# Performance work log

Measured on AMD Instinct MI355X. Metric: run time of the kernel, lower is better.

## Reference

```python
import jax, jax.numpy as jnp
import numpy as np

MARGIN = 0.7
SINKHORN_ITERS = 500


def setup_inputs() -> dict:
    key = jax.random.key(0)
    k1, k2, k3, k4, k5 = jax.random.split(key, 5)
    D, m, n = 2048, 2048, 2048
    query_features = jax.random.normal(k1, (D, m), dtype=jnp.float32)
    target_features = jax.random.normal(k2, (D, n), dtype=jnp.float32)
    # positive marginals (mu.log() / nu.log() must be finite), normalized to sum 1
    qa = jax.random.uniform(k3, (m,), dtype=jnp.float32, minval=0.1, maxval=1.0)
    ta = jax.random.uniform(k4, (n,), dtype=jnp.float32, minval=0.1, maxval=1.0)
    query_attention = qa / qa.sum()
    target_attention = ta / ta.sum()
    # contrastive label: 1 = positive pair, 0 = negative
    label = (jax.random.uniform(k5, (m,)) < 0.5).astype(jnp.float32)
    return {
        "query_features": query_features,
        "query_attention": query_attention,
        "target_features": target_features,
        "target_attention": target_attention,
        "label": label,
    }


def _pairwise_sq_dist(x, y):
    # x: [m, D], y: [n, D] -> squared euclidean distances [m, n], clamped at 0
    x2 = jnp.sum(x * x, axis=1)[:, None]
    y2 = jnp.sum(y * y, axis=1)[None, :]
    d = x2 + y2 - 2.0 * (x @ y.T)
    return jnp.maximum(d, 0.0)


def _log_sinkhorn(Z, log_mu, log_nu, iters):
    # Z: [m, n]; log-space Sinkhorn, matching torch version with batch dim squeezed
    u0 = jnp.zeros_like(log_mu)
    v0 = jnp.zeros_like(log_nu)

    def body(_, uv):
        u, v = uv
        u = log_mu - jax.nn.logsumexp(Z + v[None, :], axis=1)
        v = log_nu - jax.nn.logsumexp(Z + u[:, None], axis=0)
        return (u, v)

    u, v = jax.lax.fori_loop(0, iters, body, (u0, v0))
    return Z + u[:, None] + v[None, :]


def reference(query_features, query_attention, target_features, target_attention, label):
    qf = query_features.T  # [m, D]
    tf = target_features.T  # [n, D]
    M = _pairwise_sq_dist(qf, tf)  # [m, n]
    logP = _log_sinkhorn(M, jnp.log(query_attention), jnp.log(target_attention), SINKHORN_ITERS)
    P = jnp.exp(logP)  # [m, n]
    # per-query-descriptor residual between weighted query and OT-transported target
    resid = query_attention[:, None] * qf - P @ tf  # [m, D]
    distance = jnp.linalg.norm(resid, axis=1)  # [m]
    loss = 0.5 * label * distance ** 2 + 0.5 * (1.0 - label) * jnp.maximum(MARGIN - distance, 0.0) ** 2
    return loss.sum()
```

## Files before the change

kernel.cpp:

```cpp
#include <hip/hip_runtime.h>
#include <math.h>

#define S 2048
#define MARGIN 0.7f
#define ITERS 500

__global__ __launch_bounds__(256) void init_marg_k(const float* __restrict__ qa,
                                                   const float* __restrict__ ta,
                                                   float* __restrict__ lmu,
                                                   float* __restrict__ lnu,
                                                   float* __restrict__ vt,
                                                   float* __restrict__ dist2) {
  int i = blockIdx.x * 256 + threadIdx.x;
  lmu[i] = __logf(qa[i]);
  lnu[i] = __logf(ta[i]);
  vt[i] = 0.f;
  dist2[i] = 0.f;
}

__global__ __launch_bounds__(256) void colsumsq_k(const float* __restrict__ TF,
                                                  float* __restrict__ vt) {
  int jb = blockIdx.x & 7, dc = blockIdx.x >> 3;
  int j = jb * 256 + threadIdx.x;
  int d0 = dc * 256;
  float acc = 0.f;
  for (int d = d0; d < d0 + 256; ++d) {
    float v = TF[d * S + j];
    acc = fmaf(v, v, acc);
  }
  atomicAdd(&vt[j], acc);
}

__global__ __launch_bounds__(256) void gemm_tn_k(const float* __restrict__ A,
                                                 const float* __restrict__ B,
                                                 float* __restrict__ C, float alpha) {
  __shared__ float As[16][128];
  __shared__ float Bs[16][128];
  int t = threadIdx.x;
  int i0 = blockIdx.y * 128, j0 = blockIdx.x * 128;
  int tx = t & 15, ty = t >> 4;
  float acc[8][8];
#pragma unroll
  for (int r = 0; r < 8; ++r)
#pragma unroll
    for (int c = 0; c < 8; ++c) acc[r][c] = 0.f;

  int e = t * 4;
  int dd0 = e >> 7, ii = e & 127;
  int dd1 = dd0 + 8;
  for (int k0 = 0; k0 < S; k0 += 16) {
    float4 a0 = *(const float4*)&A[(k0 + dd0) * S + i0 + ii];
    float4 b0 = *(const float4*)&B[(k0 + dd0) * S + j0 + ii];
    float4 a1 = *(const float4*)&A[(k0 + dd1) * S + i0 + ii];
    float4 b1 = *(const float4*)&B[(k0 + dd1) * S + j0 + ii];
    __syncthreads();
    *(float4*)&As[dd0][ii] = a0; *(float4*)&Bs[dd0][ii] = b0;
    *(float4*)&As[dd1][ii] = a1; *(float4*)&Bs[dd1][ii] = b1;
    __syncthreads();
#pragma unroll
    for (int kk = 0; kk < 16; ++kk) {
      float a[8], b[8];
      *(float4*)&a[0] = *(const float4*)&As[kk][ty * 8];
      *(float4*)&a[4] = *(const float4*)&As[kk][ty * 8 + 4];
      *(float4*)&b[0] = *(const float4*)&Bs[kk][tx * 4];
      *(float4*)&b[4] = *(const float4*)&Bs[kk][64 + tx * 4];
#pragma unroll
      for (int r = 0; r < 8; ++r)
#pragma unroll
        for (int c = 0; c < 8; ++c) acc[r][c] = fmaf(a[r], b[c], acc[r][c]);
    }
  }
#pragma unroll
  for (int r = 0; r < 8; ++r) {
    int i = i0 + ty * 8 + r;
    float4 o0 = make_float4(acc[r][0] * alpha, acc[r][1] * alpha, acc[r][2] * alpha, acc[r][3] * alpha);
    float4 o1 = make_float4(acc[r][4] * alpha, acc[r][5] * alpha, acc[r][6] * alpha, acc[r][7] * alpha);
    *(float4*)&C[i * S + j0 + tx * 4] = o0;
    *(float4*)&C[i * S + j0 + 64 + tx * 4] = o1;
  }
}

__global__ __launch_bounds__(256) void transpose_k(const float* __restrict__ in,
                                                   float* __restrict__ out) {
  __shared__ float tile[64][65];
  int i0 = blockIdx.y * 64, j0 = blockIdx.x * 64;
  int tx = threadIdx.x & 63, ty = threadIdx.x >> 6;
#pragma unroll
  for (int r = 0; r < 16; ++r) {
    int row = r * 4 + ty;
    tile[row][tx] = in[(i0 + row) * S + j0 + tx];
  }
  __syncthreads();
#pragma unroll
  for (int r = 0; r < 16; ++r) {
    int row = r * 4 + ty;
    out[(j0 + row) * S + i0 + tx] = tile[tx][row];
  }
}

__global__ __launch_bounds__(256) void lse_update_k(const float* __restrict__ G,
                                                    const float* __restrict__ inPot,
                                                    const float* __restrict__ logMarg,
                                                    float* __restrict__ outPot) {
  __shared__ float red[8];
  int t = threadIdx.x;
  int row = blockIdx.x;
  const float* g = G + (size_t)row * S;
  int idx = t * 8;
  float4 g0 = *(const float4*)&g[idx];
  float4 g1 = *(const float4*)&g[idx + 4];
  float4 p0 = *(const float4*)&inPot[idx];
  float4 p1 = *(const float4*)&inPot[idx + 4];
  float v0 = g0.x + p0.x, v1 = g0.y + p0.y, v2 = g0.z + p0.z, v3 = g0.w + p0.w;
  float v4 = g1.x + p1.x, v5 = g1.y + p1.y, v6 = g1.z + p1.z, v7 = g1.w + p1.w;
  float mx = fmaxf(fmaxf(fmaxf(v0, v1), fmaxf(v2, v3)),
                   fmaxf(fmaxf(v4, v5), fmaxf(v6, v7)));
#pragma unroll
  for (int off = 32; off; off >>= 1) mx = fmaxf(mx, __shfl_xor(mx, off));
  int wave = t >> 6, lane = t & 63;
  if (lane == 0) red[wave] = mx;
  __syncthreads();
  mx = fmaxf(fmaxf(red[0], red[1]), fmaxf(red[2], red[3]));
  float s = __expf(v0 - mx) + __expf(v1 - mx) + __expf(v2 - mx) + __expf(v3 - mx) +
            __expf(v4 - mx) + __expf(v5 - mx) + __expf(v6 - mx) + __expf(v7 - mx);
#pragma unroll
  for (int off = 32; off; off >>= 1) s += __shfl_xor(s, off);
  if (lane == 0) red[4 + wave] = s;
  __syncthreads();
  if (t == 0) {
    s = red[4] + red[5] + red[6] + red[7];
    outPot[row] = logMarg[row] - (mx + __logf(s));
  }
}

__global__ __launch_bounds__(256) void rt_gemm_k(const float* __restrict__ TF,
                                                 const float* __restrict__ GpT,
                                                 const float* __restrict__ ut,
                                                 const float* __restrict__ vt,
                                                 float* __restrict__ RT) {
  __shared__ float As[16][128];
  __shared__ float Bs[16][128];
  int t = threadIdx.x;
  int d0 = blockIdx.y * 128, i0 = blockIdx.x * 128;
  int tx = t & 15, ty = t >> 4;
  float acc[8][8];
#pragma unroll
  for (int r = 0; r < 8; ++r)
#pragma unroll
    for (int c = 0; c < 8; ++c) acc[r][c] = 0.f;

  int akk = (t * 4) & 15, add0 = t >> 2;
  int eb = t * 4;
  int bkk0 = eb >> 7, bii = eb & 127, bkk1 = bkk0 + 8;
  float4 u4 = *(const float4*)&ut[i0 + bii];

  for (int k0 = 0; k0 < S; k0 += 16) {
    float4 av0 = *(const float4*)&TF[(d0 + add0) * S + k0 + akk];
    float4 av1 = *(const float4*)&TF[(d0 + add0 + 64) * S + k0 + akk];
    float4 g0 = *(const float4*)&GpT[(k0 + bkk0) * S + i0 + bii];
    float4 g1 = *(const float4*)&GpT[(k0 + bkk1) * S + i0 + bii];
    float v0 = vt[k0 + bkk0], v1 = vt[k0 + bkk1];
    __syncthreads();
    As[akk + 0][add0] = av0.x; As[akk + 1][add0] = av0.y;
    As[akk + 2][add0] = av0.z; As[akk + 3][add0] = av0.w;
    As[akk + 0][add0 + 64] = av1.x; As[akk + 1][add0 + 64] = av1.y;
    As[akk + 2][add0 + 64] = av1.z; As[akk + 3][add0 + 64] = av1.w;
    float4 p0 = make_float4(__expf(g0.x + u4.x + v0), __expf(g0.y + u4.y + v0),
                            __expf(g0.z + u4.z + v0), __expf(g0.w + u4.w + v0));
    float4 p1 = make_float4(__expf(g1.x + u4.x + v1), __expf(g1.y + u4.y + v1),
                            __expf(g1.z + u4.z + v1), __expf(g1.w + u4.w + v1));
    *(float4*)&Bs[bkk0][bii] = p0;
    *(float4*)&Bs[bkk1][bii] = p1;
    __syncthreads();
#pragma unroll
    for (int kk = 0; kk < 16; ++kk) {
      float a[8], b[8];
      *(float4*)&a[0] = *(const float4*)&As[kk][ty * 8];
      *(float4*)&a[4] = *(const float4*)&As[kk][ty * 8 + 4];
      *(float4*)&b[0] = *(const float4*)&Bs[kk][tx * 4];
      *(float4*)&b[4] = *(const float4*)&Bs[kk][64 + tx * 4];
#pragma unroll
      for (int r = 0; r < 8; ++r)
#pragma unroll
        for (int c = 0; c < 8; ++c) acc[r][c] = fmaf(a[r], b[c], acc[r][c]);
    }
  }
#pragma unroll
  for (int r = 0; r < 8; ++r) {
    int d = d0 + ty * 8 + r;
    *(float4*)&RT[d * S + i0 + tx * 4] = *(float4*)&acc[r][0];
    *(float4*)&RT[d * S + i0 + 64 + tx * 4] = *(float4*)&acc[r][4];
  }
}

__global__ __launch_bounds__(256) void dist2_partial_k(const float* __restrict__ QF,
                                                       const float* __restrict__ RT,
                                                       const float* __restrict__ qa,
                                                       float* __restrict__ dist2) {
  int ib = blockIdx.x & 7, dc = blockIdx.x >> 3;
  int i = ib * 256 + threadIdx.x;
  float qai = qa[i];
  float acc = 0.f;
  int d0 = dc * 256;
  for (int d = d0; d < d0 + 256; ++d) {
    float q = QF[d * S + i];
    float r = RT[d * S + i];
    float x = fmaf(qai, q, -r);
    acc = fmaf(x, x, acc);
  }
  atomicAdd(&dist2[i], acc);
}

__global__ __launch_bounds__(256) void loss_final_k(const float* __restrict__ dist2,
                                                    const float* __restrict__ label,
                                                    float* __restrict__ out) {
  int t = threadIdx.x;
  float acc = 0.f;
#pragma unroll
  for (int k = 0; k < 8; ++k) {
    int i = t + k * 256;
    float d2 = dist2[i];
    float dist = sqrtf(d2);
    float lab = label[i];
    float neg = fmaxf(MARGIN - dist, 0.f);
    acc += 0.5f * lab * d2 + 0.5f * (1.f - lab) * neg * neg;
  }
#pragma unroll
  for (int off = 32; off; off >>= 1) acc += __shfl_xor(acc, off);
  __shared__ float wsum[4];
  int wave = t >> 6, lane = t & 63;
  if (lane == 0) wsum[wave] = acc;
  __syncthreads();
  if (t == 0) out[0] = wsum[0] + wsum[1] + wsum[2] + wsum[3];
}

extern "C" void kernel_launch(void* const* d_in, const int* in_sizes, int n_in,
                              void* d_out, int out_size, void* d_ws, size_t ws_size,
                              hipStream_t stream) {
  const float* QF  = (const float*)d_in[0];
  const float* qa  = (const float*)d_in[1];
  const float* TF  = (const float*)d_in[2];
  const float* ta  = (const float*)d_in[3];
  const float* lab = (const float*)d_in[4];
  float* out = (float*)d_out;

  float* ws = (float*)d_ws;
  float* Gp    = ws;
  float* GpT   = Gp + S * S;
  float* ut    = GpT + S * S;
  float* vt    = ut + S;
  float* lmu   = vt + S;
  float* lnu   = lmu + S;
  float* dist2 = lnu + S;

  init_marg_k<<<8, 256, 0, stream>>>(qa, ta, lmu, lnu, vt, dist2);
  colsumsq_k<<<64, 256, 0, stream>>>(TF, vt);
  gemm_tn_k<<<dim3(16, 16), 256, 0, stream>>>(QF, TF, Gp, -2.0f);
  transpose_k<<<dim3(32, 32), 256, 0, stream>>>(Gp, GpT);

  for (int it = 0; it < ITERS; ++it) {
    lse_update_k<<<2048, 256, 0, stream>>>(Gp, vt, lmu, ut);
    lse_update_k<<<2048, 256, 0, stream>>>(GpT, ut, lnu, vt);
  }

  rt_gemm_k<<<dim3(16, 16), 256, 0, stream>>>(TF, GpT, ut, vt, Gp);
  dist2_partial_k<<<64, 256, 0, stream>>>(QF, Gp, qa, dist2);
  loss_final_k<<<1, 256, 0, stream>>>(dist2, lab, out);
}
```

Baseline: 4.542 ms.

## Replace per-iteration Sinkhorn launches with persistent cooperative kernel and LDS-resident cost rows

```diff
diff --git a/kernel.cpp b/kernel.cpp
--- a/kernel.cpp
+++ b/kernel.cpp
@@ -4,18 +4,25 @@
 #define S 2048
 #define MARGIN 0.7f
 #define ITERS 500
+#define NBLK 256
+#define TPB 512
+#define NGRP 16
 
 __global__ __launch_bounds__(256) void init_marg_k(const float* __restrict__ qa,
                                                    const float* __restrict__ ta,
                                                    float* __restrict__ lmu,
                                                    float* __restrict__ lnu,
                                                    float* __restrict__ vt,
-                                                   float* __restrict__ dist2) {
+                                                   float* __restrict__ dist2,
+                                                   unsigned* __restrict__ grp,
+                                                   unsigned* __restrict__ gbar) {
   int i = blockIdx.x * 256 + threadIdx.x;
   lmu[i] = __logf(qa[i]);
   lnu[i] = __logf(ta[i]);
   vt[i] = 0.f;
   dist2[i] = 0.f;
+  if (i < 512) grp[i] = 0u;
+  if (i == 0) *gbar = 0u;
 }
 
 __global__ __launch_bounds__(256) void colsumsq_k(const float* __restrict__ TF,
@@ -98,38 +105,127 @@
   }
 }
 
-__global__ __launch_bounds__(256) void lse_update_k(const float* __restrict__ G,
-                                                    const float* __restrict__ inPot,
-                                                    const float* __restrict__ logMarg,
-                                                    float* __restrict__ outPot) {
-  __shared__ float red[8];
-  int t = threadIdx.x;
-  int row = blockIdx.x;
-  const float* g = G + (size_t)row * S;
-  int idx = t * 8;
-  float4 g0 = *(const float4*)&g[idx];
-  float4 g1 = *(const float4*)&g[idx + 4];
-  float4 p0 = *(const float4*)&inPot[idx];
-  float4 p1 = *(const float4*)&inPot[idx + 4];
-  float v0 = g0.x + p0.x, v1 = g0.y + p0.y, v2 = g0.z + p0.z, v3 = g0.w + p0.w;
-  float v4 = g1.x + p1.x, v5 = g1.y + p1.y, v6 = g1.z + p1.z, v7 = g1.w + p1.w;
-  float mx = fmaxf(fmaxf(fmaxf(v0, v1), fmaxf(v2, v3)),
-                   fmaxf(fmaxf(v4, v5), fmaxf(v6, v7)));
-#pragma unroll
-  for (int off = 32; off; off >>= 1) mx = fmaxf(mx, __shfl_xor(mx, off));
-  int wave = t >> 6, lane = t & 63;
-  if (lane == 0) red[wave] = mx;
-  __syncthreads();
-  mx = fmaxf(fmaxf(red[0], red[1]), fmaxf(red[2], red[3]));
-  float s = __expf(v0 - mx) + __expf(v1 - mx) + __expf(v2 - mx) + __expf(v3 - mx) +
-            __expf(v4 - mx) + __expf(v5 - mx) + __expf(v6 - mx) + __expf(v7 - mx);
+#define PADD(P, A) P.x += A.x; P.y += A.y; P.z += A.z; P.w += A.w
+#define PMAX(P) fmaxf(fmaxf(P.x, P.y), fmaxf(P.z, P.w))
+#define PEXPS(P) (__expf(P.x - m) + __expf(P.y - m) + __expf(P.z - m) + __expf(P.w - m))
+
+__device__ __forceinline__ void stage_pot(const float* __restrict__ src,
+                                          float* __restrict__ s_pot, int t) {
+  const unsigned long long* s64 = (const unsigned long long*)src;
+  unsigned long long* d64 = (unsigned long long*)s_pot;
+#pragma unroll
+  for (int k = 0; k < 2; ++k) {
+    int idx = t + (k << 9);
+    d64[idx] = __hip_atomic_load(&s64[idx], __ATOMIC_RELAXED,
+                                 __HIP_MEMORY_SCOPE_AGENT);
+  }
+}
+
+__device__ __forceinline__ float lse_row(const float* __restrict__ grow,
+                                         const float* __restrict__ s_pot,
+                                         int lane) {
+  int j0 = lane << 2;
+  float4 p0 = *(const float4*)&s_pot[j0];
+  float4 p1 = *(const float4*)&s_pot[j0 + 256];
+  float4 p2 = *(const float4*)&s_pot[j0 + 512];
+  float4 p3 = *(const float4*)&s_pot[j0 + 768];
+  float4 p4 = *(const float4*)&s_pot[j0 + 1024];
+  float4 p5 = *(const float4*)&s_pot[j0 + 1280];
+  float4 p6 = *(const float4*)&s_pot[j0 + 1536];
+  float4 p7 = *(const float4*)&s_pot[j0 + 1792];
+  float4 a0 = *(const float4*)&grow[j0];
+  float4 a1 = *(const float4*)&grow[j0 + 256];
+  float4 a2 = *(const float4*)&grow[j0 + 512];
+  float4 a3 = *(const float4*)&grow[j0 + 768];
+  float4 a4 = *(const float4*)&grow[j0 + 1024];
+  float4 a5 = *(const float4*)&grow[j0 + 1280];
+  float4 a6 = *(const float4*)&grow[j0 + 1536];
+  float4 a7 = *(const float4*)&grow[j0 + 1792];
+  PADD(p0, a0); PADD(p1, a1); PADD(p2, a2); PADD(p3, a3);
+  PADD(p4, a4); PADD(p5, a5); PADD(p6, a6); PADD(p7, a7);
+  float m0 = PMAX(p0), m1 = PMAX(p1), m2 = PMAX(p2), m3 = PMAX(p3);
+  float m4 = PMAX(p4), m5 = PMAX(p5), m6 = PMAX(p6), m7 = PMAX(p7);
+  m0 = fmaxf(m0, m1); m2 = fmaxf(m2, m3); m4 = fmaxf(m4, m5); m6 = fmaxf(m6, m7);
+  float m = fmaxf(fmaxf(m0, m2), fmaxf(m4, m6));
+#pragma unroll
+  for (int off = 32; off; off >>= 1) m = fmaxf(m, __shfl_xor(m, off));
+  float s = PEXPS(p0) + PEXPS(p1) + PEXPS(p2) + PEXPS(p3) +
+            PEXPS(p4) + PEXPS(p5) + PEXPS(p6) + PEXPS(p7);
 #pragma unroll
   for (int off = 32; off; off >>= 1) s += __shfl_xor(s, off);
-  if (lane == 0) red[4 + wave] = s;
-  __syncthreads();
-  if (t == 0) {
-    s = red[4] + red[5] + red[6] + red[7];
-    outPot[row] = logMarg[row] - (mx + __logf(s));
+  return m + __logf(s);
+}
+
+__device__ __forceinline__ void gridbar(unsigned* __restrict__ grp,
+                                        unsigned* __restrict__ gbar,
+                                        int g, unsigned ph) {
+  __syncthreads();
+  if (threadIdx.x == 0) {
+    unsigned old = __hip_atomic_fetch_add(&grp[g * 32], 1u, __ATOMIC_RELAXED,
+                                          __HIP_MEMORY_SCOPE_AGENT);
+    if ((old & (NGRP - 1)) == NGRP - 1)
+      __hip_atomic_fetch_add(gbar, 1u, __ATOMIC_RELAXED, __HIP_MEMORY_SCOPE_AGENT);
+    unsigned tgt = (ph + 1u) * NGRP;
+    while (__hip_atomic_load(gbar, __ATOMIC_RELAXED, __HIP_MEMORY_SCOPE_AGENT) < tgt)
+      __builtin_amdgcn_s_sleep(1);
+  }
+  __syncthreads();
+}
+
+__global__ __launch_bounds__(TPB) void sinkhorn_k(
+    const float* __restrict__ Gp, const float* __restrict__ GpT,
+    const float* __restrict__ lmu, const float* __restrict__ lnu,
+    float* __restrict__ ut, float* __restrict__ vt,
+    unsigned* __restrict__ grp, unsigned* __restrict__ gbar) {
+  __shared__ float s_gu[8 * S];
+  __shared__ float s_gv[8 * S];
+  __shared__ float s_pot[S];
+
+  const int t = threadIdx.x;
+  const int wv = t >> 6, lane = t & 63;
+  const int bid = blockIdx.x;
+  const int row = (bid << 3) + wv;
+  const int g = bid & (NGRP - 1);
+
+  {
+    const float* gu = Gp + (size_t)row * S;
+    const float* gv = GpT + (size_t)row * S;
+    float* lgu = s_gu + wv * S;
+    float* lgv = s_gv + wv * S;
+#pragma unroll
+    for (int c = 0; c < 8; ++c) {
+      int j = (lane << 2) + (c << 8);
+      *(float4*)&lgu[j] = *(const float4*)&gu[j];
+      *(float4*)&lgv[j] = *(const float4*)&gv[j];
+    }
+  }
+  const float lmu_r = lmu[row];
+  const float lnu_r = lnu[row];
+  const float* grow_u = s_gu + wv * S;
+  const float* grow_v = s_gv + wv * S;
+  unsigned ph = 0;
+  __syncthreads();
+
+  for (int it = 0; it < ITERS; ++it) {
+    stage_pot(vt, s_pot, t);
+    __syncthreads();
+    {
+      float nv = lmu_r - lse_row(grow_u, s_pot, lane);
+      if (lane == 0)
+        __hip_atomic_store(&ut[row], nv, __ATOMIC_RELAXED,
+                           __HIP_MEMORY_SCOPE_AGENT);
+    }
+    gridbar(grp, gbar, g, ph); ++ph;
+
+    stage_pot(ut, s_pot, t);
+    __syncthreads();
+    {
+      float nv = lnu_r - lse_row(grow_v, s_pot, lane);
+      if (lane == 0)
+        __hip_atomic_store(&vt[row], nv, __ATOMIC_RELAXED,
+                           __HIP_MEMORY_SCOPE_AGENT);
+    }
+    gridbar(grp, gbar, g, ph); ++ph;
   }
 }
 
@@ -252,15 +348,22 @@
   float* lmu   = vt + S;
   float* lnu   = lmu + S;
   float* dist2 = lnu + S;
-
-  init_marg_k<<<8, 256, 0, stream>>>(qa, ta, lmu, lnu, vt, dist2);
+  unsigned* grp  = (unsigned*)(dist2 + S);
+  unsigned* gbar = grp + 512;
+
+  init_marg_k<<<8, 256, 0, stream>>>(qa, ta, lmu, lnu, vt, dist2, grp, gbar);
   colsumsq_k<<<64, 256, 0, stream>>>(TF, vt);
   gemm_tn_k<<<dim3(16, 16), 256, 0, stream>>>(QF, TF, Gp, -2.0f);
   transpose_k<<<dim3(32, 32), 256, 0, stream>>>(Gp, GpT);
 
-  for (int it = 0; it < ITERS; ++it) {
-    lse_update_k<<<2048, 256, 0, stream>>>(Gp, vt, lmu, ut);
-    lse_update_k<<<2048, 256, 0, stream>>>(GpT, ut, lnu, vt);
+  {
+    const float* cGp = Gp; const float* cGpT = GpT;
+    const float* clmu = lmu; const float* clnu = lnu;
+    float* cut = ut; float* cvt = vt;
+    unsigned* cgrp = grp; unsigned* cgbar = gbar;
+    void* kargs[] = {&cGp, &cGpT, &clmu, &clnu, &cut, &cvt, &cgrp, &cgbar};
+    hipLaunchCooperativeKernel((const void*)sinkhorn_k, dim3(NBLK), dim3(TPB),
+                               kargs, 0, stream);
   }
 
   rt_gemm_k<<<dim3(16, 16), 256, 0, stream>>>(TF, GpT, ut, vt, Gp);
```

New measurement: 5.241 ms. +15.4%, slower.
